# Kernel tuning notes

Hardware: AMD Instinct MI355X
Metric: run time of the kernel (lower is better)

The kernel has to match this reference:

```python
import jax, jax.numpy as jnp
import numpy as np

BETA = 0.5
LAMBDA = 0.5
EPS = 1e-24


def setup_inputs() -> dict:
    key = jax.random.key(0)
    k1, k2 = jax.random.split(key)
    seq = jax.random.normal(k1, (32, 512, 128), dtype=jnp.float32)
    fism_items = jax.random.normal(k2, (32, 2048, 128), dtype=jnp.float32)
    return {"seq": seq, "fism_items": fism_items}


def reference(seq, fism_items):
    # scores: [B, L, N]
    w = jnp.einsum('bld,bnd->bln', seq, fism_items)
    w_shift = w - jnp.max(w, axis=-1, keepdims=True)
    exp_w = jnp.exp(w_shift)
    exp_sum = jnp.sum(exp_w, axis=-1, keepdims=True)
    if BETA != 1.0:
        exp_sum = jnp.power(exp_sum, jnp.float32(BETA))
    att = exp_w / (exp_sum + EPS)  # power-normalized softmax
    att_vecs = jnp.einsum('bln,bnd->bld', att, fism_items)
    if LAMBDA < 1:
        return seq * (1.0 - LAMBDA) + seq * att_vecs * LAMBDA
    return seq * att_vecs
```

## Files before the change

kernel.cpp:

```cpp
#include <hip/hip_runtime.h>
#include <hip/hip_bf16.h>
#include <math.h>

typedef _Float16 half8  __attribute__((ext_vector_type(8)));
typedef _Float16 half2v __attribute__((ext_vector_type(2)));
typedef __fp16   fp16x2 __attribute__((ext_vector_type(2)));
typedef float    f32x4  __attribute__((ext_vector_type(4)));

#define DDIM 128
#define LQ   512
#define NKV  2048
#define KVB  32
#define NIT  16

union U32H2 { unsigned u; fp16x2 h; };
union H8W   { unsigned u[4]; half8 h; };

__device__ __forceinline__ int swzk(int row) { return (row & 7) << 3; }
__device__ __forceinline__ int swzv(int d)   { return ((d ^ (d >> 4)) & 3) << 3; }

__global__ __launch_bounds__(512, 4)
void gattn(const float* __restrict__ seq, const float* __restrict__ fism,
           float* __restrict__ out)
{
  const int tid  = threadIdx.x;
  const int lane = tid & 63;
  const int wv   = tid >> 6;
  const int wq   = wv & 1;
  const int kvq  = wv >> 1;
  const int q16  = lane & 15;
  const int g    = lane >> 4;

  const int swz = (blockIdx.x & 7) * 64 + (blockIdx.x >> 3);
  const int b   = swz >> 4;
  const int qb  = (swz & 15) * 32;

  const float* seqB = seq  + (size_t)b * LQ * DDIM;
  const float* fisB = fism + (size_t)b * NKV * DDIM;
  float*       outB = out  + (size_t)b * LQ * DDIM;

  __shared__ _Float16 Ksh[4][KVB * DDIM];
  __shared__ _Float16 VTsh[4][DDIM * KVB];
  __shared__ float    stats[4][2][16][3];

  half8 qf[4];
  {
    const int qrow = qb + wq * 16 + q16;
    #pragma unroll
    for (int c = 0; c < 4; ++c) {
      const float* p = seqB + (size_t)qrow * DDIM + c * 32 + g * 8;
      float4 a  = *(const float4*)p;
      float4 b2 = *(const float4*)(p + 4);
      half8 h;
      h[0]=(_Float16)a.x;  h[1]=(_Float16)a.y;  h[2]=(_Float16)a.z;  h[3]=(_Float16)a.w;
      h[4]=(_Float16)b2.x; h[5]=(_Float16)b2.y; h[6]=(_Float16)b2.z; h[7]=(_Float16)b2.w;
      qf[c] = h;
    }
  }

  const int sp   = tid >> 3;
  const int dgrp = tid & 7;
  const int qstg = sp >> 4;
  const int spc  = sp & 15;

  f32x4 acc[8];
  #pragma unroll
  for (int i = 0; i < 8; ++i) { f32x4 z = {0.f,0.f,0.f,0.f}; acc[i] = z; }

  float m_run = -INFINITY, tmax = -INFINITY, S_run = 0.f;

  auto write_stage = [&](const float4* v) {
    #pragma unroll
    for (int r = 0; r < 2; ++r) {
      const int row = 2*spc + r;
      #pragma unroll
      for (int hh = 0; hh < 2; ++hh) {
        const float4 x = v[r*4 + hh*2];
        const float4 y = v[r*4 + hh*2 + 1];
        half8 h;
        h[0]=(_Float16)x.x; h[1]=(_Float16)x.y; h[2]=(_Float16)x.z; h[3]=(_Float16)x.w;
        h[4]=(_Float16)y.x; h[5]=(_Float16)y.y; h[6]=(_Float16)y.z; h[7]=(_Float16)y.w;
        const int idx = row*DDIM + ((dgrp*16 + hh*8) ^ swzk(row));
        *(half8*)&Ksh[qstg][idx] = h;
      }
    }
    #pragma unroll
    for (int k = 0; k < 16; ++k) {
      const int d = dgrp*16 + k;
      half2v pk;
      pk[0] = (_Float16)(((const float*)&v[k>>2])[k&3]);
      pk[1] = (_Float16)(((const float*)&v[4 + (k>>2)])[k&3]);
      const int idx = d*KVB + ((2*spc) ^ swzv(d));
      *(half2v*)&VTsh[qstg][idx] = pk;
    }
  };

  auto load_glb = [&](float4* v, int t) {
    const float* src = fisB + (size_t)(qstg*(NKV/4) + t*KVB) * DDIM;
    #pragma unroll
    for (int r = 0; r < 2; ++r)
      #pragma unroll
      for (int k = 0; k < 4; ++k)
        v[r*4+k] = *(const float4*)(src + (size_t)(2*spc + r)*DDIM + dgrp*16 + k*4);
  };

  {
    float4 stg[8];
    load_glb(stg, 0);
    write_stage(stg);
  }

  for (int t = 0; t < NIT; ++t) {
    __syncthreads();
    float4 nxt[8];
    const bool have = (t + 1 < NIT);
    if (have) load_glb(nxt, t + 1);

    f32x4 sv[2];
    #pragma unroll
    for (int ns = 0; ns < 2; ++ns) {
      f32x4 x = {0.f,0.f,0.f,0.f};
      const int row = ns*16 + q16;
      #pragma unroll
      for (int c = 0; c < 4; ++c) {
        const int idx = row*DDIM + ((c*32 + g*8) ^ swzk(row));
        half8 kf = *(const half8*)&Ksh[kvq][idx];
        x = __builtin_amdgcn_mfma_f32_16x16x32_f16(kf, qf[c], x, 0, 0, 0);
      }
      sv[ns] = x;
    }

    float cmax = sv[0][0];
    #pragma unroll
    for (int ns = 0; ns < 2; ++ns)
      #pragma unroll
      for (int i = 0; i < 4; ++i)
        cmax = fmaxf(cmax, sv[ns][i]);
    cmax = fmaxf(cmax, __shfl_xor(cmax, 16));
    cmax = fmaxf(cmax, __shfl_xor(cmax, 32));
    tmax = fmaxf(tmax, cmax);
    if (__any(cmax > m_run + 8.f)) {
      const float mn = fmaxf(m_run, cmax);
      const float sc = __expf(m_run - mn);
      S_run *= sc;
      m_run = mn;
      const float s0 = __shfl(sc, (g<<4) | (4*g + 0));
      const float s1 = __shfl(sc, (g<<4) | (4*g + 1));
      const float s2 = __shfl(sc, (g<<4) | (4*g + 2));
      const float s3 = __shfl(sc, (g<<4) | (4*g + 3));
      const f32x4 scv = {s0, s1, s2, s3};
      #pragma unroll
      for (int dsu = 0; dsu < 8; ++dsu) acc[dsu] *= scv;
    }
    float lsum = 0.f;
    #pragma unroll
    for (int ns = 0; ns < 2; ++ns)
      #pragma unroll
      for (int i = 0; i < 4; ++i) {
        const float p = __expf(sv[ns][i] - m_run);
        sv[ns][i] = p;
        lsum += p;
      }
    lsum += __shfl_xor(lsum, 16);
    lsum += __shfl_xor(lsum, 32);
    S_run += lsum;

    unsigned upk[2][2];
    #pragma unroll
    for (int ns = 0; ns < 2; ++ns) {
      U32H2 u0, u1;
      u0.h = __builtin_amdgcn_cvt_pkrtz(sv[ns][0], sv[ns][1]);
      u1.h = __builtin_amdgcn_cvt_pkrtz(sv[ns][2], sv[ns][3]);
      upk[ns][0] = u0.u; upk[ns][1] = u1.u;
    }
    {
      H8W aw;
      #pragma unroll
      for (int tt = 0; tt < 4; ++tt) {
        const int src = q16 + 16 * ((g & 1) * 2 + (tt >> 1));
        const unsigned lo = (unsigned)__shfl((int)upk[0][tt & 1], src);
        const unsigned hi = (unsigned)__shfl((int)upk[1][tt & 1], src);
        aw.u[tt] = (g < 2) ? lo : hi;
      }
      const half8 pa = aw.h;
      #pragma unroll
      for (int dsu = 0; dsu < 8; ++dsu) {
        const int d = dsu*16 + q16;
        const int idx = d*KVB + ((g*8) ^ swzv(d));
        half8 vf = *(const half8*)&VTsh[kvq][idx];
        acc[dsu] = __builtin_amdgcn_mfma_f32_16x16x32_f16(pa, vf, acc[dsu], 0, 0, 0);
      }
    }

    __syncthreads();
    if (have) write_stage(nxt);
  }

  __syncthreads();
  if (kvq != 0) {
    const int rgn = (kvq - 1) * 2 + wq;
    float* base = (rgn < 4) ? ((float*)&Ksh[0][0]  + rgn * 2048)
                            : ((float*)&VTsh[0][0] + (rgn - 4) * 2048);
    float* p = base + lane * 32;
    #pragma unroll
    for (int dsu = 0; dsu < 8; ++dsu)
      *(f32x4*)&p[dsu*4] = acc[dsu];
    if (g == 0) {
      stats[kvq][wq][q16][0] = m_run;
      stats[kvq][wq][q16][1] = S_run;
      stats[kvq][wq][q16][2] = tmax;
    }
  }
  __syncthreads();

  if (kvq == 0) {
    float mj[4], Sj[4], tj[4];
    mj[0] = m_run; Sj[0] = S_run; tj[0] = tmax;
    #pragma unroll
    for (int j = 1; j < 4; ++j) {
      mj[j] = stats[j][wq][q16][0];
      Sj[j] = stats[j][wq][q16][1];
      tj[j] = stats[j][wq][q16][2];
    }
    const float M = fmaxf(fmaxf(tj[0], tj[1]), fmaxf(tj[2], tj[3]));
    float aj[4], den = 0.f;
    #pragma unroll
    for (int j = 0; j < 4; ++j) { aj[j] = __expf(mj[j] - M); den += aj[j] * Sj[j]; }
    const float rs = rsqrtf(den);
    float fr[4][4];
    #pragma unroll
    for (int j = 0; j < 4; ++j) {
      const float fj = aj[j] * rs;
      #pragma unroll
      for (int i = 0; i < 4; ++i)
        fr[j][i] = __shfl(fj, (g<<4) | (4*g + i));
    }
    #pragma unroll
    for (int dsu = 0; dsu < 8; ++dsu) {
      f32x4 av = acc[dsu];
      av *= (f32x4){fr[0][0], fr[0][1], fr[0][2], fr[0][3]};
      #pragma unroll
      for (int j = 1; j < 4; ++j) {
        const int rgn = (j - 1) * 2 + wq;
        const float* base = (rgn < 4) ? ((const float*)&Ksh[0][0]  + rgn * 2048)
                                      : ((const float*)&VTsh[0][0] + (rgn - 4) * 2048);
        const f32x4 pj = *(const f32x4*)&base[lane*32 + dsu*4];
        av += pj * (f32x4){fr[j][0], fr[j][1], fr[j][2], fr[j][3]};
      }
      #pragma unroll
      for (int i = 0; i < 4; ++i) {
        const int qrow = qb + wq*16 + 4*g + i;
        const int d = dsu*16 + q16;
        const float s = seqB[(size_t)qrow * DDIM + d];
        outB[(size_t)qrow * DDIM + d] = 0.5f * s * (1.f + av[i]);
      }
    }
  }
}

extern "C" void kernel_launch(void* const* d_in, const int* in_sizes, int n_in,
                              void* d_out, int out_size, void* d_ws, size_t ws_size,
                              hipStream_t stream) {
  const float* seq  = (const float*)d_in[0];
  const float* fism = (const float*)d_in[1];
  float* out = (float*)d_out;
  gattn<<<dim3(512), dim3(512), 0, stream>>>(seq, fism, out);
}
```

Before: 62.29 us.

## Double query rows per block and widen KV tile to reuse staged K/V

Each block now handles 64 query rows (two 16-row sub-tiles per wave) and stages 64 KV rows per iteration. Each staged K/V fragment then feeds two MFMAs, and the grid is halved, so the fp32-to-fp16 conversion and global loading of fism is done half as often across the grid. The cost is double the LDS (about 128KB), more registers, occupancy bounds lowered to 2, and only 256 blocks, so fewer waves are available to hide latency. The reduction buffer also gains an XOR swizzle to cut bank conflicts.

```diff
diff --git a/kernel.cpp b/kernel.cpp
--- a/kernel.cpp
+++ b/kernel.cpp
@@ -3,23 +3,23 @@
 #include <math.h>
 
 typedef _Float16 half8  __attribute__((ext_vector_type(8)));
-typedef _Float16 half2v __attribute__((ext_vector_type(2)));
+typedef _Float16 half4v __attribute__((ext_vector_type(4)));
 typedef __fp16   fp16x2 __attribute__((ext_vector_type(2)));
 typedef float    f32x4  __attribute__((ext_vector_type(4)));
 
 #define DDIM 128
 #define LQ   512
 #define NKV  2048
-#define KVB  32
-#define NIT  16
+#define KVB  64
+#define NIT  8
 
 union U32H2 { unsigned u; fp16x2 h; };
 union H8W   { unsigned u[4]; half8 h; };
 
 __device__ __forceinline__ int swzk(int row) { return (row & 7) << 3; }
-__device__ __forceinline__ int swzv(int d)   { return ((d ^ (d >> 4)) & 3) << 3; }
-
-__global__ __launch_bounds__(512, 4)
+__device__ __forceinline__ int swzv(int d)   { return ((d ^ (d >> 4)) & 7) << 3; }
+
+__global__ __launch_bounds__(512, 2)
 void gattn(const float* __restrict__ seq, const float* __restrict__ fism,
            float* __restrict__ out)
 {
@@ -31,9 +31,9 @@
   const int q16  = lane & 15;
   const int g    = lane >> 4;
 
-  const int swz = (blockIdx.x & 7) * 64 + (blockIdx.x >> 3);
-  const int b   = swz >> 4;
-  const int qb  = (swz & 15) * 32;
+  const int swz = (blockIdx.x & 7) * 32 + (blockIdx.x >> 3);
+  const int b   = swz >> 3;
+  const int qb  = (swz & 7) * 64;
 
   const float* seqB = seq  + (size_t)b * LQ * DDIM;
   const float* fisB = fism + (size_t)b * NKV * DDIM;
@@ -41,11 +41,12 @@
 
   __shared__ _Float16 Ksh[4][KVB * DDIM];
   __shared__ _Float16 VTsh[4][DDIM * KVB];
-  __shared__ float    stats[4][2][16][3];
-
-  half8 qf[4];
-  {
-    const int qrow = qb + wq * 16 + q16;
+  __shared__ float    stats[4][2][2][16][3];
+
+  half8 qf[2][4];
+  #pragma unroll
+  for (int qs = 0; qs < 2; ++qs) {
+    const int qrow = qb + wq * 32 + qs * 16 + q16;
     #pragma unroll
     for (int c = 0; c < 4; ++c) {
       const float* p = seqB + (size_t)qrow * DDIM + c * 32 + g * 8;
@@ -54,7 +55,7 @@
       half8 h;
       h[0]=(_Float16)a.x;  h[1]=(_Float16)a.y;  h[2]=(_Float16)a.z;  h[3]=(_Float16)a.w;
       h[4]=(_Float16)b2.x; h[5]=(_Float16)b2.y; h[6]=(_Float16)b2.z; h[7]=(_Float16)b2.w;
-      qf[c] = h;
+      qf[qs][c] = h;
     }
   }
 
@@ -63,16 +64,20 @@
   const int qstg = sp >> 4;
   const int spc  = sp & 15;
 
-  f32x4 acc[8];
+  f32x4 acc[2][8];
   #pragma unroll
-  for (int i = 0; i < 8; ++i) { f32x4 z = {0.f,0.f,0.f,0.f}; acc[i] = z; }
-
-  float m_run = -INFINITY, tmax = -INFINITY, S_run = 0.f;
+  for (int qs = 0; qs < 2; ++qs)
+    #pragma unroll
+    for (int i = 0; i < 8; ++i) { f32x4 z = {0.f,0.f,0.f,0.f}; acc[qs][i] = z; }
+
+  float m_run[2] = {-INFINITY, -INFINITY};
+  float tmax[2]  = {-INFINITY, -INFINITY};
+  float S_run[2] = {0.f, 0.f};
 
   auto write_stage = [&](const float4* v) {
     #pragma unroll
-    for (int r = 0; r < 2; ++r) {
-      const int row = 2*spc + r;
+    for (int r = 0; r < 4; ++r) {
+      const int row = 4*spc + r;
       #pragma unroll
       for (int hh = 0; hh < 2; ++hh) {
         const float4 x = v[r*4 + hh*2];
@@ -87,108 +92,119 @@
     #pragma unroll
     for (int k = 0; k < 16; ++k) {
       const int d = dgrp*16 + k;
-      half2v pk;
-      pk[0] = (_Float16)(((const float*)&v[k>>2])[k&3]);
-      pk[1] = (_Float16)(((const float*)&v[4 + (k>>2)])[k&3]);
-      const int idx = d*KVB + ((2*spc) ^ swzv(d));
-      *(half2v*)&VTsh[qstg][idx] = pk;
+      half4v pk;
+      #pragma unroll
+      for (int r = 0; r < 4; ++r)
+        pk[r] = (_Float16)(((const float*)&v[r*4 + (k>>2)])[k&3]);
+      const int idx = d*KVB + ((4*spc) ^ swzv(d));
+      *(half4v*)&VTsh[qstg][idx] = pk;
     }
   };
 
   auto load_glb = [&](float4* v, int t) {
     const float* src = fisB + (size_t)(qstg*(NKV/4) + t*KVB) * DDIM;
     #pragma unroll
-    for (int r = 0; r < 2; ++r)
+    for (int r = 0; r < 4; ++r)
       #pragma unroll
       for (int k = 0; k < 4; ++k)
-        v[r*4+k] = *(const float4*)(src + (size_t)(2*spc + r)*DDIM + dgrp*16 + k*4);
+        v[r*4+k] = *(const float4*)(src + (size_t)(4*spc + r)*DDIM + dgrp*16 + k*4);
   };
 
   {
-    float4 stg[8];
+    float4 stg[16];
     load_glb(stg, 0);
     write_stage(stg);
   }
 
   for (int t = 0; t < NIT; ++t) {
     __syncthreads();
-    float4 nxt[8];
+    float4 nxt[16];
     const bool have = (t + 1 < NIT);
     if (have) load_glb(nxt, t + 1);
 
-    f32x4 sv[2];
-    #pragma unroll
-    for (int ns = 0; ns < 2; ++ns) {
-      f32x4 x = {0.f,0.f,0.f,0.f};
+    f32x4 sv[2][4];
+    #pragma unroll
+    for (int ns = 0; ns < 4; ++ns) {
+      f32x4 x0 = {0.f,0.f,0.f,0.f}, x1 = {0.f,0.f,0.f,0.f};
       const int row = ns*16 + q16;
       #pragma unroll
       for (int c = 0; c < 4; ++c) {
         const int idx = row*DDIM + ((c*32 + g*8) ^ swzk(row));
         half8 kf = *(const half8*)&Ksh[kvq][idx];
-        x = __builtin_amdgcn_mfma_f32_16x16x32_f16(kf, qf[c], x, 0, 0, 0);
-      }
-      sv[ns] = x;
-    }
-
-    float cmax = sv[0][0];
-    #pragma unroll
-    for (int ns = 0; ns < 2; ++ns)
-      #pragma unroll
-      for (int i = 0; i < 4; ++i)
-        cmax = fmaxf(cmax, sv[ns][i]);
-    cmax = fmaxf(cmax, __shfl_xor(cmax, 16));
-    cmax = fmaxf(cmax, __shfl_xor(cmax, 32));
-    tmax = fmaxf(tmax, cmax);
-    if (__any(cmax > m_run + 8.f)) {
-      const float mn = fmaxf(m_run, cmax);
-      const float sc = __expf(m_run - mn);
-      S_run *= sc;
-      m_run = mn;
-      const float s0 = __shfl(sc, (g<<4) | (4*g + 0));
-      const float s1 = __shfl(sc, (g<<4) | (4*g + 1));
-      const float s2 = __shfl(sc, (g<<4) | (4*g + 2));
-      const float s3 = __shfl(sc, (g<<4) | (4*g + 3));
-      const f32x4 scv = {s0, s1, s2, s3};
-      #pragma unroll
-      for (int dsu = 0; dsu < 8; ++dsu) acc[dsu] *= scv;
-    }
-    float lsum = 0.f;
-    #pragma unroll
-    for (int ns = 0; ns < 2; ++ns)
-      #pragma unroll
-      for (int i = 0; i < 4; ++i) {
-        const float p = __expf(sv[ns][i] - m_run);
-        sv[ns][i] = p;
-        lsum += p;
-      }
-    lsum += __shfl_xor(lsum, 16);
-    lsum += __shfl_xor(lsum, 32);
-    S_run += lsum;
-
-    unsigned upk[2][2];
-    #pragma unroll
-    for (int ns = 0; ns < 2; ++ns) {
-      U32H2 u0, u1;
-      u0.h = __builtin_amdgcn_cvt_pkrtz(sv[ns][0], sv[ns][1]);
-      u1.h = __builtin_amdgcn_cvt_pkrtz(sv[ns][2], sv[ns][3]);
-      upk[ns][0] = u0.u; upk[ns][1] = u1.u;
-    }
-    {
-      H8W aw;
+        x0 = __builtin_amdgcn_mfma_f32_16x16x32_f16(kf, qf[0][c], x0, 0, 0, 0);
+        x1 = __builtin_amdgcn_mfma_f32_16x16x32_f16(kf, qf[1][c], x1, 0, 0, 0);
+      }
+      sv[0][ns] = x0; sv[1][ns] = x1;
+    }
+
+    unsigned upk[2][4][2];
+    #pragma unroll
+    for (int qs = 0; qs < 2; ++qs) {
+      float cmax = sv[qs][0][0];
+      #pragma unroll
+      for (int ns = 0; ns < 4; ++ns)
+        #pragma unroll
+        for (int i = 0; i < 4; ++i)
+          cmax = fmaxf(cmax, sv[qs][ns][i]);
+      cmax = fmaxf(cmax, __shfl_xor(cmax, 16));
+      cmax = fmaxf(cmax, __shfl_xor(cmax, 32));
+      tmax[qs] = fmaxf(tmax[qs], cmax);
+      if (__any(cmax > m_run[qs] + 8.f)) {
+        const float mn = fmaxf(m_run[qs], cmax);
+        const float sc = __expf(m_run[qs] - mn);
+        S_run[qs] *= sc;
+        m_run[qs] = mn;
+        const float s0 = __shfl(sc, (g<<4) | (4*g + 0));
+        const float s1 = __shfl(sc, (g<<4) | (4*g + 1));
+        const float s2 = __shfl(sc, (g<<4) | (4*g + 2));
+        const float s3 = __shfl(sc, (g<<4) | (4*g + 3));
+        const f32x4 scv = {s0, s1, s2, s3};
+        #pragma unroll
+        for (int dsu = 0; dsu < 8; ++dsu) acc[qs][dsu] *= scv;
+      }
+      float lsum = 0.f;
+      #pragma unroll
+      for (int ns = 0; ns < 4; ++ns)
+        #pragma unroll
+        for (int i = 0; i < 4; ++i) {
+          const float p = __expf(sv[qs][ns][i] - m_run[qs]);
+          sv[qs][ns][i] = p;
+          lsum += p;
+        }
+      lsum += __shfl_xor(lsum, 16);
+      lsum += __shfl_xor(lsum, 32);
+      S_run[qs] += lsum;
+
+      #pragma unroll
+      for (int ns = 0; ns < 4; ++ns) {
+        U32H2 u0, u1;
+        u0.h = __builtin_amdgcn_cvt_pkrtz(sv[qs][ns][0], sv[qs][ns][1]);
+        u1.h = __builtin_amdgcn_cvt_pkrtz(sv[qs][ns][2], sv[qs][ns][3]);
+        upk[qs][ns][0] = u0.u; upk[qs][ns][1] = u1.u;
+      }
+    }
+
+    #pragma unroll
+    for (int c = 0; c < 2; ++c) {
+      H8W aw0, aw1;
       #pragma unroll
       for (int tt = 0; tt < 4; ++tt) {
         const int src = q16 + 16 * ((g & 1) * 2 + (tt >> 1));
-        const unsigned lo = (unsigned)__shfl((int)upk[0][tt & 1], src);
-        const unsigned hi = (unsigned)__shfl((int)upk[1][tt & 1], src);
-        aw.u[tt] = (g < 2) ? lo : hi;
-      }
-      const half8 pa = aw.h;
+        const unsigned lo0 = (unsigned)__shfl((int)upk[0][2*c  ][tt & 1], src);
+        const unsigned hi0 = (unsigned)__shfl((int)upk[0][2*c+1][tt & 1], src);
+        const unsigned lo1 = (unsigned)__shfl((int)upk[1][2*c  ][tt & 1], src);
+        const unsigned hi1 = (unsigned)__shfl((int)upk[1][2*c+1][tt & 1], src);
+        aw0.u[tt] = (g < 2) ? lo0 : hi0;
+        aw1.u[tt] = (g < 2) ? lo1 : hi1;
+      }
+      const half8 pa0 = aw0.h, pa1 = aw1.h;
       #pragma unroll
       for (int dsu = 0; dsu < 8; ++dsu) {
         const int d = dsu*16 + q16;
-        const int idx = d*KVB + ((g*8) ^ swzv(d));
+        const int idx = d*KVB + ((c*32 + g*8) ^ swzv(d));
         half8 vf = *(const half8*)&VTsh[kvq][idx];
-        acc[dsu] = __builtin_amdgcn_mfma_f32_16x16x32_f16(pa, vf, acc[dsu], 0, 0, 0);
+        acc[0][dsu] = __builtin_amdgcn_mfma_f32_16x16x32_f16(pa0, vf, acc[0][dsu], 0, 0, 0);
+        acc[1][dsu] = __builtin_amdgcn_mfma_f32_16x16x32_f16(pa1, vf, acc[1][dsu], 0, 0, 0);
       }
     }
 
@@ -197,62 +213,69 @@
   }
 
   __syncthreads();
+
+  float* Kf  = (float*)&Ksh[0][0];
+  float* VTf = (float*)&VTsh[0][0];
   if (kvq != 0) {
-    const int rgn = (kvq - 1) * 2 + wq;
-    float* base = (rgn < 4) ? ((float*)&Ksh[0][0]  + rgn * 2048)
-                            : ((float*)&VTsh[0][0] + (rgn - 4) * 2048);
-    float* p = base + lane * 32;
-    #pragma unroll
-    for (int dsu = 0; dsu < 8; ++dsu)
-      *(f32x4*)&p[dsu*4] = acc[dsu];
-    if (g == 0) {
-      stats[kvq][wq][q16][0] = m_run;
-      stats[kvq][wq][q16][1] = S_run;
-      stats[kvq][wq][q16][2] = tmax;
+    #pragma unroll
+    for (int qs = 0; qs < 2; ++qs) {
+      const int rgn = (((kvq - 1) * 2 + wq) << 1) | qs;
+      float* base = (rgn < 8) ? (Kf + rgn * 2048) : (VTf + (rgn - 8) * 2048);
+      float* p = base + lane * 32;
+      #pragma unroll
+      for (int dsu = 0; dsu < 8; ++dsu)
+        *(f32x4*)&p[(dsu * 4) ^ ((lane & 7) << 2)] = acc[qs][dsu];
+      if (g == 0) {
+        stats[kvq][wq][qs][q16][0] = m_run[qs];
+        stats[kvq][wq][qs][q16][1] = S_run[qs];
+        stats[kvq][wq][qs][q16][2] = tmax[qs];
+      }
     }
   }
   __syncthreads();
 
   if (kvq == 0) {
-    float mj[4], Sj[4], tj[4];
-    mj[0] = m_run; Sj[0] = S_run; tj[0] = tmax;
-    #pragma unroll
-    for (int j = 1; j < 4; ++j) {
-      mj[j] = stats[j][wq][q16][0];
-      Sj[j] = stats[j][wq][q16][1];
-      tj[j] = stats[j][wq][q16][2];
-    }
-    const float M = fmaxf(fmaxf(tj[0], tj[1]), fmaxf(tj[2], tj[3]));
-    float aj[4], den = 0.f;
-    #pragma unroll
-    for (int j = 0; j < 4; ++j) { aj[j] = __expf(mj[j] - M); den += aj[j] * Sj[j]; }
-    const float rs = rsqrtf(den);
-    float fr[4][4];
-    #pragma unroll
-    for (int j = 0; j < 4; ++j) {
-      const float fj = aj[j] * rs;
-      #pragma unroll
-      for (int i = 0; i < 4; ++i)
-        fr[j][i] = __shfl(fj, (g<<4) | (4*g + i));
-    }
-    #pragma unroll
-    for (int dsu = 0; dsu < 8; ++dsu) {
-      f32x4 av = acc[dsu];
-      av *= (f32x4){fr[0][0], fr[0][1], fr[0][2], fr[0][3]};
+    #pragma unroll
+    for (int qs = 0; qs < 2; ++qs) {
+      float mj[4], Sj[4], tj[4];
+      mj[0] = m_run[qs]; Sj[0] = S_run[qs]; tj[0] = tmax[qs];
       #pragma unroll
       for (int j = 1; j < 4; ++j) {
-        const int rgn = (j - 1) * 2 + wq;
-        const float* base = (rgn < 4) ? ((const float*)&Ksh[0][0]  + rgn * 2048)
-                                      : ((const float*)&VTsh[0][0] + (rgn - 4) * 2048);
-        const f32x4 pj = *(const f32x4*)&base[lane*32 + dsu*4];
-        av += pj * (f32x4){fr[j][0], fr[j][1], fr[j][2], fr[j][3]};
-      }
-      #pragma unroll
-      for (int i = 0; i < 4; ++i) {
-        const int qrow = qb + wq*16 + 4*g + i;
-        const int d = dsu*16 + q16;
-        const float s = seqB[(size_t)qrow * DDIM + d];
-        outB[(size_t)qrow * DDIM + d] = 0.5f * s * (1.f + av[i]);
+        mj[j] = stats[j][wq][qs][q16][0];
+        Sj[j] = stats[j][wq][qs][q16][1];
+        tj[j] = stats[j][wq][qs][q16][2];
+      }
+      const float M = fmaxf(fmaxf(tj[0], tj[1]), fmaxf(tj[2], tj[3]));
+      float aj[4], den = 0.f;
+      #pragma unroll
+      for (int j = 0; j < 4; ++j) { aj[j] = __expf(mj[j] - M); den += aj[j] * Sj[j]; }
+      const float rs = rsqrtf(den);
+      float fr[4][4];
+      #pragma unroll
+      for (int j = 0; j < 4; ++j) {
+        const float fj = aj[j] * rs;
+        #pragma unroll
+        for (int i = 0; i < 4; ++i)
+          fr[j][i] = __shfl(fj, (g<<4) | (4*g + i));
+      }
+      #pragma unroll
+      for (int dsu = 0; dsu < 8; ++dsu) {
+        f32x4 av = acc[qs][dsu];
+        av *= (f32x4){fr[0][0], fr[0][1], fr[0][2], fr[0][3]};
+        #pragma unroll
+        for (int j = 1; j < 4; ++j) {
+          const int rgn = (((j - 1) * 2 + wq) << 1) | qs;
+          const float* base = (rgn < 8) ? (Kf + rgn * 2048) : (VTf + (rgn - 8) * 2048);
+          const f32x4 pj = *(const f32x4*)&base[lane*32 + ((dsu * 4) ^ ((lane & 7) << 2))];
+          av += pj * (f32x4){fr[j][0], fr[j][1], fr[j][2], fr[j][3]};
+        }
+        #pragma unroll
+        for (int i = 0; i < 4; ++i) {
+          const int qrow = qb + wq*32 + qs*16 + 4*g + i;
+          const int d = dsu*16 + q16;
+          const float s = seqB[(size_t)qrow * DDIM + d];
+          outB[(size_t)qrow * DDIM + d] = 0.5f * s * (1.f + av[i]);
+        }
       }
     }
   }
@@ -264,5 +287,5 @@
   const float* seq  = (const float*)d_in[0];
   const float* fism = (const float*)d_in[1];
   float* out = (float*)d_out;
-  gattn<<<dim3(512), dim3(512), 0, stream>>>(seq, fism, out);
+  gattn<<<dim3(256), dim3(512), 0, stream>>>(seq, fism, out);
 }
```

New measurement: 52.41 us. 1.19x faster.
